# Optimization experiments

Measured on AMD Instinct MI355X. Metric: run time of the kernel, lower is better.

Reference implementation:

```python
import jax, jax.numpy as jnp
import numpy as np
import math

D_MODEL = 512
NHEAD = 8
DH = D_MODEL // NHEAD
TEMP = math.sqrt(D_MODEL / NHEAD)
EPS = 1e-5


def setup_inputs() -> dict:
    key = jax.random.key(0)
    ks = jax.random.split(key, 16)
    d, f = D_MODEL, 2 * D_MODEL
    s = 1.0 / math.sqrt(d)
    inp = {
        "x": jax.random.normal(ks[0], (1024, 16, d), dtype=jnp.float32),
        # attention projections (stored [in, out]; y = x @ W + b)
        "Wq": jax.random.normal(ks[1], (d, d), jnp.float32) * s,
        "bq": jax.random.normal(ks[2], (d,), jnp.float32) * 0.01,
        "Wk": jax.random.normal(ks[3], (d, d), jnp.float32) * s,
        "bk": jax.random.normal(ks[4], (d,), jnp.float32) * 0.01,
        "Wv": jax.random.normal(ks[5], (d, d), jnp.float32) * s,
        "bv": jax.random.normal(ks[6], (d,), jnp.float32) * 0.01,
        # layernorms
        "g1": jnp.ones((d,), jnp.float32),
        "be1": jnp.zeros((d,), jnp.float32),
        "g2": jnp.ones((d,), jnp.float32),
        "be2": jnp.zeros((d,), jnp.float32),
        # FFN
        "W1": jax.random.normal(ks[7], (d, f), jnp.float32) * s,
        "bf1": jax.random.normal(ks[8], (f,), jnp.float32) * 0.01,
        "W2": jax.random.normal(ks[9], (f, d), jnp.float32) * (1.0 / math.sqrt(f)),
        "bf2": jax.random.normal(ks[10], (d,), jnp.float32) * 0.01,
    }
    return inp


def _ln(x, g, b):
    m = jnp.mean(x, axis=-1, keepdims=True)
    v = jnp.var(x, axis=-1, keepdims=True)
    return (x - m) * jax.lax.rsqrt(v + EPS) * g + b


def reference(x, Wq, bq, Wk, bk, Wv, bv, g1, be1, g2, be2, W1, bf1, W2, bf2):
    A, B, d = x.shape
    x = _ln(x, g1, be1)                       # [A,B,d]
    # project then move batch axis first: [B,A,H,dh] -> [B,H,A,dh]
    def proj(W, b):
        y = jnp.swapaxes(x @ W + b, 0, 1)      # [B,A,d]
        return y.reshape(B, A, NHEAD, DH).transpose(0, 2, 1, 3)
    q, k, v = proj(Wq, bq), proj(Wk, bk), proj(Wv, bv)
    scores = jnp.einsum("bhqd,bhkd->bhqk", q, k)          # [B,H,A,A]
    # per-head global std over (B,A,A), unbiased (torch.std default ddof=1)
    std = jnp.std(scores, axis=(0, 2, 3), ddof=1)          # [H]
    scaling = TEMP * jnp.sqrt(1.0 + std)                   # [H]
    attn = jax.nn.softmax(scores / scaling[None, :, None, None], axis=-1)
    out = jnp.einsum("bhqk,bhkd->bhqd", attn, v)           # [B,H,A,dh]
    out = jnp.swapaxes(out.transpose(0, 2, 1, 3).reshape(B, A, d), 0, 1)  # [A,B,d]
    xt = _ln(x + out, g2, be2)
    h = jax.nn.gelu(xt @ W1 + bf1, approximate=False)      # exact GELU (torch default)
    return xt + h @ W2 + bf2
```

## Files before the change

### kernel.cpp

```cpp
#include <hip/hip_runtime.h>
#include <stdint.h>

typedef unsigned short u16;
typedef u16 u16x4 __attribute__((ext_vector_type(4)));
typedef unsigned int u32x4 __attribute__((ext_vector_type(4)));
typedef float f32x4 __attribute__((ext_vector_type(4)));
typedef float f32x16 __attribute__((ext_vector_type(16)));
typedef __bf16 bf16x8 __attribute__((ext_vector_type(8)));

#define DEVI __device__ __forceinline__

DEVI u16 f2bf(float f) {
  uint32_t u = __builtin_bit_cast(uint32_t, f);
  u = (u + 0x7FFFu + ((u >> 16) & 1u)) >> 16;
  return (u16)u;
}
DEVI float bf2f(u16 h) {
  uint32_t u = ((uint32_t)h) << 16;
  return __builtin_bit_cast(float, u);
}
DEVI f32x4 mfma16(u32x4 a, u32x4 b, f32x4 c) {
  return __builtin_amdgcn_mfma_f32_16x16x32_bf16(
      __builtin_bit_cast(bf16x8, a), __builtin_bit_cast(bf16x8, b), c, 0, 0, 0);
}
DEVI f32x16 mfma32(u32x4 a, u32x4 b, f32x16 c) {
  return __builtin_amdgcn_mfma_f32_32x32x16_bf16(
      __builtin_bit_cast(bf16x8, a), __builtin_bit_cast(bf16x8, b), c, 0, 0, 0);
}
DEVI uint32_t cvtpk(float lo, float hi) {
  uint32_t w;
  asm("v_cvt_pk_bf16_f32 %0, %1, %2" : "=v"(w) : "v"(lo), "v"(hi));
  return w;
}
DEVI void plswap(uint32_t& a, uint32_t& b) {
  asm("v_permlane32_swap_b32 %0, %1" : "+v"(a), "+v"(b));
}
DEVI float xmax2(float v) {
  uint32_t a = __builtin_bit_cast(uint32_t, v), b = a;
  plswap(a, b);
  return fmaxf(__builtin_bit_cast(float, a), __builtin_bit_cast(float, b));
}

#define AS1 __attribute__((address_space(1)))
#define AS3 __attribute__((address_space(3)))
DEVI void gload16(const void* g, void* l) {
  __builtin_amdgcn_global_load_lds((AS1 void*)(uintptr_t)g,
                                   (AS3 void*)(uint32_t)(uintptr_t)l, 16, 0, 0);
}

DEVI float wred(float v) {
#pragma unroll
  for (int m = 1; m < 64; m <<= 1) v += __shfl_xor(v, m);
  return v;
}

__global__ __launch_bounds__(256) void k_prep_ln1(
    const float* __restrict__ Wq, const float* __restrict__ Wk,
    const float* __restrict__ Wv, const float* __restrict__ W1,
    const float* __restrict__ W2, const float* __restrict__ x,
    const float* __restrict__ gam, const float* __restrict__ bet,
    u16* __restrict__ wqkv_t, u16* __restrict__ w1t, u16* __restrict__ w2t,
    u16* __restrict__ xn_res) {
  __shared__ float tile[64][65];
  int bid = blockIdx.x, tid = threadIdx.x;
  if (bid < 448) {
    const float* W;
    u16* Wt;
    int Kr, Nc, n0, k0;
    if (bid < 192) {
      int w = bid / 64, t = bid & 63;
      W = (w == 0) ? Wq : (w == 1) ? Wk : Wv;
      Wt = wqkv_t + (size_t)w * 512 * 512;
      Kr = 512; Nc = 512; n0 = (t & 7) * 64; k0 = (t >> 3) * 64;
    } else if (bid < 320) {
      int t = bid - 192;
      W = W1; Wt = w1t;
      Kr = 512; Nc = 1024; n0 = (t & 15) * 64; k0 = (t >> 4) * 64;
    } else {
      int t = bid - 320;
      W = W2; Wt = w2t;
      Kr = 1024; Nc = 512; n0 = (t & 7) * 64; k0 = (t >> 3) * 64;
    }
#pragma unroll
    for (int i = 0; i < 16; i++) {
      int idx = i * 256 + tid;
      int r = idx >> 6, cc = idx & 63;
      tile[r][cc] = W[(size_t)(k0 + r) * Nc + n0 + cc];
    }
    __syncthreads();
#pragma unroll
    for (int i = 0; i < 16; i++) {
      int idx = i * 256 + tid;
      int r = idx >> 6, cc = idx & 63;
      Wt[(size_t)(n0 + r) * Kr + k0 + cc] = f2bf(tile[cc][r]);
    }
  } else {
    int wid = tid >> 6, lane = tid & 63;
    int row = (bid - 448) * 4 + wid;
    const float* xr = x + (size_t)row * 512 + lane * 8;
    f32x4 v0 = *(const f32x4*)xr;
    f32x4 v1 = *(const f32x4*)(xr + 4);
    float s = 0.f, ss = 0.f;
#pragma unroll
    for (int j = 0; j < 4; j++) {
      s += v0[j] + v1[j];
      ss += v0[j] * v0[j] + v1[j] * v1[j];
    }
    s = wred(s);
    ss = wred(ss);
    float mean = s * (1.0f / 512.0f);
    float var = ss * (1.0f / 512.0f) - mean * mean;
    float rstd = rsqrtf(var + 1e-5f);
    const float* gp = gam + lane * 8;
    const float* bp = bet + lane * 8;
    f32x4 ga = *(const f32x4*)gp, gb = *(const f32x4*)(gp + 4);
    f32x4 ba = *(const f32x4*)bp, bb = *(const f32x4*)(bp + 4);
    u16x4 o0, o1;
#pragma unroll
    for (int j = 0; j < 4; j++) {
      o0[j] = f2bf((v0[j] - mean) * rstd * ga[j] + ba[j]);
      o1[j] = f2bf((v1[j] - mean) * rstd * gb[j] + bb[j]);
    }
    u16* pr = xn_res + (size_t)row * 512 + lane * 8;
    *(u16x4*)pr = o0;
    *(u16x4*)(pr + 4) = o1;
  }
}

__global__ __launch_bounds__(256) void k_ln2(const u16* __restrict__ xn,
                                             const u16* __restrict__ ao,
                                             const float* __restrict__ gam,
                                             const float* __restrict__ bet,
                                             u16* __restrict__ xt) {
  int tid = threadIdx.x, wid = tid >> 6, lane = tid & 63;
  int row = blockIdx.x * 4 + wid;
  size_t base = (size_t)row * 512 + lane * 8;
  u16x4 a0 = *(const u16x4*)&xn[base], a1 = *(const u16x4*)&xn[base + 4];
  u16x4 c0 = *(const u16x4*)&ao[base], c1 = *(const u16x4*)&ao[base + 4];
  float v[8];
#pragma unroll
  for (int j = 0; j < 4; j++) {
    v[j] = bf2f(a0[j]) + bf2f(c0[j]);
    v[4 + j] = bf2f(a1[j]) + bf2f(c1[j]);
  }
  float s = 0.f, ss = 0.f;
#pragma unroll
  for (int j = 0; j < 8; j++) {
    s += v[j];
    ss += v[j] * v[j];
  }
  s = wred(s);
  ss = wred(ss);
  float mean = s * (1.0f / 512.0f);
  float var = ss * (1.0f / 512.0f) - mean * mean;
  float rstd = rsqrtf(var + 1e-5f);
  const float* gp = gam + lane * 8;
  const float* bp = bet + lane * 8;
  u16x4 o0, o1;
#pragma unroll
  for (int j = 0; j < 4; j++) {
    o0[j] = f2bf((v[j] - mean) * rstd * gp[j] + bp[j]);
    o1[j] = f2bf((v[4 + j] - mean) * rstd * gp[4 + j] + bp[4 + j]);
  }
  u16* pr = xt + base;
  *(u16x4*)pr = o0;
  *(u16x4*)(pr + 4) = o1;
}

template <int EPI, int BM>
__global__ __launch_bounds__(256, BM == 64 ? 4 : 3) void k_gemm(
    const u16* __restrict__ A, const u16* __restrict__ B, int K,
    const float* __restrict__ b0, const float* __restrict__ b1,
    const float* __restrict__ b2, u16* __restrict__ o0, u16* __restrict__ o1,
    u16* __restrict__ o2, u16* __restrict__ qt, u16* __restrict__ kt,
    const u16* __restrict__ resid, float* __restrict__ outf) {
  constexpr int MI = BM / 64;
  __shared__ __align__(16) u16 As[BM * 64];
  __shared__ __align__(16) u16 Bs[128 * 64];
  const int tid = threadIdx.x;
  const int wid = tid >> 6, lane = tid & 63;
  const int r31 = lane & 31, hi = lane >> 5;
  const int m0 = blockIdx.x * BM, n0 = blockIdx.y * 128;
  const int wr = (wid >> 1) * (BM / 2), wc = (wid & 1) * 64;
  const int srow = tid >> 3, scb = tid & 7;

  f32x16 acc[MI][2];
#pragma unroll
  for (int i = 0; i < MI; i++)
#pragma unroll
    for (int j = 0; j < 2; j++)
#pragma unroll
      for (int e = 0; e < 16; e++) acc[i][j][e] = 0.f;

  auto stage = [&](int k0) {
#pragma unroll
    for (int i = 0; i < BM / 32; i++) {
      int row = i * 32 + srow;
      int col = ((scb ^ (row & 7)) << 3);
      const u16* asrc;
      if constexpr (EPI == 0) {
        int m = m0 + row;
        asrc = A + ((size_t)(((m & 1023) << 4) | (m >> 10))) * K + k0 + col;
      } else {
        asrc = A + (size_t)(m0 + row) * K + k0 + col;
      }
      gload16(asrc, &As[(i * 256 + tid) * 8]);
    }
#pragma unroll
    for (int i = 0; i < 4; i++) {
      int row = i * 32 + srow;
      int col = ((scb ^ (row & 7)) << 3);
      gload16(B + (size_t)(n0 + row) * K + k0 + col, &Bs[(i * 256 + tid) * 8]);
    }
  };

  for (int k0 = 0; k0 < K; k0 += 64) {
    __syncthreads();
    stage(k0);
    __syncthreads();
#pragma unroll
    for (int kk = 0; kk < 4; kk++) {
      u32x4 af[MI], bfr[2];
#pragma unroll
      for (int mi = 0; mi < MI; mi++) {
        int row = wr + mi * 32 + r31;
        int cb = (kk * 2 + hi) ^ (row & 7);
        af[mi] = *(const u32x4*)&As[row * 64 + cb * 8];
      }
#pragma unroll
      for (int ni = 0; ni < 2; ni++) {
        int row = wc + ni * 32 + r31;
        int cb = (kk * 2 + hi) ^ (row & 7);
        bfr[ni] = *(const u32x4*)&Bs[row * 64 + cb * 8];
      }
#pragma unroll
      for (int mi = 0; mi < MI; mi++)
#pragma unroll
        for (int ni = 0; ni < 2; ni++)
          acc[mi][ni] = mfma32(af[mi], bfr[ni], acc[mi][ni]);
    }
  }

  if constexpr (EPI == 0) {
#pragma unroll
    for (int mi = 0; mi < MI; mi++) {
#pragma unroll
      for (int ni = 0; ni < 2; ni++) {
        int n = n0 + wc + ni * 32 + r31;
        int which = n >> 9, h = (n >> 6) & 7, dh = n & 63;
        const float* bp = (which == 0) ? b0 : (which == 1) ? b1 : b2;
        float bias = bp[n & 511];
#pragma unroll
        for (int grp = 0; grp < 4; grp++) {
          int mbase = m0 + wr + mi * 32 + grp * 8 + hi * 4;
          int bb = mbase >> 10, aa = mbase & 1023;
          int bh = bb * 8 + h;
          u16x4 pk;
#pragma unroll
          for (int j = 0; j < 4; j++) pk[j] = f2bf(acc[mi][ni][grp * 4 + j] + bias);
          if (which < 2) {
            u16* dstr = ((which == 0) ? o0 : o1) + ((size_t)bh * 1024 + aa) * 64 + dh;
#pragma unroll
            for (int j = 0; j < 4; j++) dstr[(size_t)j * 64] = pk[j];
            u16* dstt = ((which == 0) ? qt : kt) + ((size_t)bh * 64 + dh) * 1024 + aa;
            *(u16x4*)dstt = pk;
          } else {
            *(u16x4*)(o2 + ((size_t)bh * 64 + dh) * 1024 + aa) = pk;
          }
        }
      }
    }
  } else if constexpr (EPI == 1) {
#pragma unroll
    for (int mi = 0; mi < MI; mi++) {
#pragma unroll
      for (int ni = 0; ni < 2; ni++) {
        int n = n0 + wc + ni * 32 + r31;
        float bias = b0[n];
#pragma unroll
        for (int i = 0; i < 16; i++) {
          int m = m0 + wr + mi * 32 + (i & 3) + 8 * (i >> 2) + 4 * hi;
          float v = acc[mi][ni][i] + bias;
          v = 0.5f * v * (1.0f + erff(v * 0.70710678118654752f));
          o0[(size_t)m * 1024 + n] = f2bf(v);
        }
      }
    }
  } else {
#pragma unroll
    for (int mi = 0; mi < MI; mi++) {
#pragma unroll
      for (int ni = 0; ni < 2; ni++) {
        int n = n0 + wc + ni * 32 + r31;
        float bias = b0[n];
#pragma unroll
        for (int i = 0; i < 16; i++) {
          int m = m0 + wr + mi * 32 + (i & 3) + 8 * (i >> 2) + 4 * hi;
          float v = acc[mi][ni][i] + bias + bf2f(resid[(size_t)m * 512 + n]);
          outf[(size_t)m * 512 + n] = v;
        }
      }
    }
  }
}

__global__ __launch_bounds__(256) void k_gram2(const u16* __restrict__ qt,
                                               const u16* __restrict__ kt,
                                               float* __restrict__ stats) {
  __shared__ __align__(16) u16 Xq[2][64 * 64];
  __shared__ __align__(16) u16 Xk[2][64 * 64];
  __shared__ float red[8];
  int tid = threadIdx.x, wid = tid >> 6, lane = tid & 63;
  int g = lane >> 4, c = lane & 15;
  int bh = blockIdx.x;
  const int srow = tid >> 3, scb = tid & 7;
  const u32x4 ones = {0x3F803F80u, 0x3F803F80u, 0x3F803F80u, 0x3F803F80u};
  const f32x4 zero = {0.f, 0.f, 0.f, 0.f};
  const u16* qsrc = qt + ((size_t)bh << 16);
  const u16* ksrc = kt + ((size_t)bh << 16);

  f32x4 gq[4], gk[4], csq = zero, csk = zero;
#pragma unroll
  for (int j = 0; j < 4; j++) {
    gq[j] = zero;
    gk[j] = zero;
  }

  auto stage = [&](int buf, int k0) {
#pragma unroll
    for (int i = 0; i < 2; i++) {
      int row = i * 32 + srow;
      int col = ((scb ^ (row & 7)) << 3);
      gload16(qsrc + (size_t)row * 1024 + k0 + col, &Xq[buf][(i * 256 + tid) * 8]);
      gload16(ksrc + (size_t)row * 1024 + k0 + col, &Xk[buf][(i * 256 + tid) * 8]);
    }
  };

  stage(0, 0);
  int cur = 0;
  for (int k0 = 0; k0 < 1024; k0 += 64) {
    __syncthreads();
    if (k0 + 64 < 1024) stage(cur ^ 1, k0 + 64);
#pragma unroll
    for (int kk = 0; kk < 2; kk++) {
      int arow = wid * 16 + c;
      int cba = (kk * 4 + g) ^ (arow & 7);
      u32x4 aq = *(const u32x4*)&Xq[cur][arow * 64 + cba * 8];
      u32x4 ak = *(const u32x4*)&Xk[cur][arow * 64 + cba * 8];
      csq = mfma16(aq, ones, csq);
      csk = mfma16(ak, ones, csk);
#pragma unroll
      for (int ni = 0; ni < 4; ni++) {
        int brow = ni * 16 + c;
        int cbb = (kk * 4 + g) ^ (brow & 7);
        u32x4 bq = *(const u32x4*)&Xq[cur][brow * 64 + cbb * 8];
        u32x4 bk = *(const u32x4*)&Xk[cur][brow * 64 + cbb * 8];
        gq[ni] = mfma16(aq, bq, gq[ni]);
        gk[ni] = mfma16(ak, bk, gk[ni]);
      }
    }
    cur ^= 1;
  }
  float part = 0.f;
#pragma unroll
  for (int ni = 0; ni < 4; ni++)
#pragma unroll
    for (int r = 0; r < 4; r++) part += gq[ni][r] * gk[ni][r];
  part = wred(part);
  float cpart = 0.f;
  if (c == 0) {
#pragma unroll
    for (int r = 0; r < 4; r++) cpart += csq[r] * csk[r];
  }
  cpart = wred(cpart);
  if (lane == 0) {
    red[wid] = part;
    red[4 + wid] = cpart;
  }
  __syncthreads();
  if (tid == 0) {
    stats[bh * 2] = red[0] + red[1] + red[2] + red[3];
    stats[bh * 2 + 1] = red[4] + red[5] + red[6] + red[7];
  }
}

__global__ __launch_bounds__(256, 3) void k_attn(const u16* __restrict__ q,
                                                 const u16* __restrict__ k,
                                                 const u16* __restrict__ vt,
                                                 const float* __restrict__ stats,
                                                 u16* __restrict__ ao) {
  __shared__ __align__(16) u16 Ks[2][64 * 64];
  __shared__ __align__(16) u16 Vs[2][64 * 64];
  int tid = threadIdx.x, wid = tid >> 6, lane = tid & 63;
  int r = lane & 31, hi = lane >> 5, h8 = hi * 8;
  int bh = blockIdx.x, qt = blockIdx.y;
  int b = bh >> 3, h = bh & 7;
  float ssq = 0.f, sm = 0.f;
#pragma unroll
  for (int bb2 = 0; bb2 < 16; bb2++) {
    ssq += stats[(bb2 * 8 + h) * 2];
    sm += stats[(bb2 * 8 + h) * 2 + 1];
  }
  const float NN = 16777216.0f;
  float var = (ssq - sm * sm / NN) / (NN - 1.0f);
  float sd = sqrtf(fmaxf(var, 0.0f));
  float sc = 1.4426950408889634f / (8.0f * sqrtf(1.0f + sd));
  int q0 = qt * 128 + wid * 32;
  const u16* qb = q + ((size_t)bh << 16);
  const u16* kb = k + ((size_t)bh << 16);
  const u16* vb = vt + ((size_t)bh << 16);
  const int srow = tid >> 3, scb = tid & 7;
  const u32x4 ones = {0x3F803F80u, 0x3F803F80u, 0x3F803F80u, 0x3F803F80u};

  u32x4 qf[4];
  const u16* qrow = qb + (size_t)(q0 + r) * 64 + h8;
#pragma unroll
  for (int ks = 0; ks < 4; ks++) {
    u32x4 raw = *(const u32x4*)(qrow + ks * 16);
    u32x4 w;
#pragma unroll
    for (int t = 0; t < 4; t++) {
      float lo = bf2f((u16)(raw[t] & 0xffffu)) * sc;
      float hi_ = bf2f((u16)(raw[t] >> 16)) * sc;
      w[t] = cvtpk(lo, hi_);
    }
    qf[ks] = w;
  }

  const f32x16 zero16 = {0.f, 0.f, 0.f, 0.f, 0.f, 0.f, 0.f, 0.f,
                         0.f, 0.f, 0.f, 0.f, 0.f, 0.f, 0.f, 0.f};
  f32x16 o0 = zero16, o1 = zero16, lacc = zero16;
  float m_run = -1e30f;

  auto stage = [&](int buf, int t0) {
#pragma unroll
    for (int i = 0; i < 2; i++) {
      int row = i * 32 + srow;
      int col = ((scb ^ (row & 7)) << 3);
      gload16(kb + (size_t)(t0 + row) * 64 + col, &Ks[buf][(i * 256 + tid) * 8]);
      gload16(vb + (size_t)row * 1024 + t0 + col, &Vs[buf][(i * 256 + tid) * 8]);
    }
  };

  stage(0, 0);
  int cur = 0;
  for (int t0 = 0; t0 < 1024; t0 += 64) {
    __syncthreads();
    if (t0 + 64 < 1024) stage(cur ^ 1, t0 + 64);
    const u16* Kc = Ks[cur];
    const u16* Vc = Vs[cur];
#pragma unroll
    for (int ss = 0; ss < 2; ss++) {
      f32x16 st = zero16;
      int rk = ss * 32 + r;
      __builtin_amdgcn_s_setprio(1);
#pragma unroll
      for (int ks = 0; ks < 4; ks++) {
        int cb = (ks * 2 + hi) ^ (rk & 7);
        u32x4 kf = *(const u32x4*)&Kc[rk * 64 + cb * 8];
        st = mfma32(kf, qf[ks], st);
      }
      __builtin_amdgcn_s_setprio(0);
      float mx[8];
#pragma unroll
      for (int i = 0; i < 8; i++) mx[i] = fmaxf(st[i], st[i + 8]);
#pragma unroll
      for (int i = 0; i < 4; i++) mx[i] = fmaxf(mx[i], mx[i + 4]);
      float pm = fmaxf(fmaxf(mx[0], mx[2]), fmaxf(mx[1], mx[3]));
      pm = xmax2(pm);
      if (__any(pm > m_run + 8.0f)) {
        float mnew = fmaxf(m_run, pm);
        float al = exp2f(m_run - mnew);
        lacc[0] *= al;
#pragma unroll
        for (int i = 0; i < 16; i++) {
          o0[i] *= al;
          o1[i] *= al;
        }
        m_run = mnew;
      }
      float p[16];
#pragma unroll
      for (int i = 0; i < 16; i++) p[i] = exp2f(st[i] - m_run);
      __builtin_amdgcn_s_setprio(1);
#pragma unroll
      for (int ks = 0; ks < 2; ks++) {
        uint32_t A0 = cvtpk(p[ks * 8 + 0], p[ks * 8 + 1]);
        uint32_t A1 = cvtpk(p[ks * 8 + 4], p[ks * 8 + 5]);
        plswap(A0, A1);
        uint32_t B0 = cvtpk(p[ks * 8 + 2], p[ks * 8 + 3]);
        uint32_t B1 = cvtpk(p[ks * 8 + 6], p[ks * 8 + 7]);
        plswap(B0, B1);
        u32x4 pa = {A0, B0, A1, B1};
        lacc = mfma32(ones, pa, lacc);
#pragma unroll
        for (int mt = 0; mt < 2; mt++) {
          int rv = mt * 32 + r;
          int cb = (ss * 4 + ks * 2 + hi) ^ (rv & 7);
          u32x4 vf = *(const u32x4*)&Vc[rv * 64 + cb * 8];
          if (mt == 0)
            o0 = mfma32(vf, pa, o0);
          else
            o1 = mfma32(vf, pa, o1);
        }
      }
      __builtin_amdgcn_s_setprio(0);
    }
    cur ^= 1;
  }

  float inv = 1.0f / lacc[0];
  int a_idx = q0 + r;
  u16* aop = ao + ((size_t)(a_idx * 16 + b)) * 512 + h * 64;
#pragma unroll
  for (int i = 0; i < 16; i++) {
    int dh0 = (i & 3) + 8 * (i >> 2) + 4 * hi;
    aop[dh0] = f2bf(o0[i] * inv);
    aop[32 + dh0] = f2bf(o1[i] * inv);
  }
}

extern "C" void kernel_launch(void* const* d_in, const int* in_sizes, int n_in,
                              void* d_out, int out_size, void* d_ws, size_t ws_size,
                              hipStream_t stream) {
  const float* x = (const float*)d_in[0];
  const float* Wq = (const float*)d_in[1];
  const float* bq = (const float*)d_in[2];
  const float* Wk = (const float*)d_in[3];
  const float* bk = (const float*)d_in[4];
  const float* Wv = (const float*)d_in[5];
  const float* bv = (const float*)d_in[6];
  const float* g1 = (const float*)d_in[7];
  const float* be1 = (const float*)d_in[8];
  const float* g2 = (const float*)d_in[9];
  const float* be2 = (const float*)d_in[10];
  const float* W1 = (const float*)d_in[11];
  const float* bf1 = (const float*)d_in[12];
  const float* W2 = (const float*)d_in[13];
  const float* bf2v = (const float*)d_in[14];
  float* out = (float*)d_out;

  char* w = (char*)d_ws;
  size_t off = 0;
  auto alloc = [&](size_t bytes) -> void* {
    void* p = w + off;
    off += (bytes + 255) & ~(size_t)255;
    return p;
  };
  u16* xn_res = (u16*)alloc(16384ull * 512 * 2);
  u16* qbuf = (u16*)alloc(128ull * 1024 * 64 * 2);
  u16* kbuf = (u16*)alloc(128ull * 1024 * 64 * 2);
  u16* vtb = (u16*)alloc(128ull * 64 * 1024 * 2);
  u16* qtb = (u16*)alloc(128ull * 64 * 1024 * 2);
  u16* ktb = (u16*)alloc(128ull * 64 * 1024 * 2);
  u16* wqkv_t = (u16*)alloc(1536ull * 512 * 2);
  u16* w1t = (u16*)alloc(1024ull * 512 * 2);
  u16* w2t = (u16*)alloc(512ull * 1024 * 2);
  u16* h_bf = (u16*)alloc(16384ull * 1024 * 2);
  float* stats = (float*)alloc(128ull * 2 * 4);
  u16* ao_bf = (u16*)alloc(16384ull * 512 * 2);
  u16* xt_bf = (u16*)alloc(16384ull * 512 * 2);

  k_prep_ln1<<<448 + 4096, 256, 0, stream>>>(Wq, Wk, Wv, W1, W2, x, g1, be1,
                                             wqkv_t, w1t, w2t, xn_res);

  k_gemm<0, 128><<<dim3(128, 12), 256, 0, stream>>>(
      xn_res, wqkv_t, 512, bq, bk, bv, qbuf, kbuf, vtb, qtb, ktb, nullptr,
      nullptr);

  k_gram2<<<128, 256, 0, stream>>>(qtb, ktb, stats);

  k_attn<<<dim3(128, 8), 256, 0, stream>>>(qbuf, kbuf, vtb, stats, ao_bf);

  k_ln2<<<4096, 256, 0, stream>>>(xn_res, ao_bf, g2, be2, xt_bf);

  k_gemm<1, 128><<<dim3(128, 8), 256, 0, stream>>>(
      xt_bf, w1t, 512, bf1, nullptr, nullptr, h_bf, nullptr, nullptr, nullptr,
      nullptr, nullptr, nullptr);
  k_gemm<2, 64><<<dim3(256, 4), 256, 0, stream>>>(
      h_bf, w2t, 1024, bf2v, nullptr, nullptr, nullptr, nullptr, nullptr,
      nullptr, nullptr, xt_bf, out);
  (void)in_sizes; (void)n_in; (void)out_size; (void)ws_size;
}
```

Measured before the change: 214.1 us.

## Process two query tiles per attention wave and remap GEMM blocks across XCDs

The attention kernel now has each wave handle two 32-row query tiles. Each K fragment loaded from LDS is reused for two QK^T MFMAs, and each V fragment for two PV MFMAs. The grid is halved and occupancy lowered to 2 blocks per CU to make room for the extra accumulators. The GEMMs switch to a 1D grid with an XCD-aware block remap, so consecutive tiles share the L2 on one XCD. exp2f is also replaced by the hardware exp2 builtin. The attention change trades more registers and fewer resident waves for less LDS traffic per MFMA.

```diff
diff --git a/kernel.cpp b/kernel.cpp
--- a/kernel.cpp
+++ b/kernel.cpp
@@ -40,6 +40,7 @@
   plswap(a, b);
   return fmaxf(__builtin_bit_cast(float, a), __builtin_bit_cast(float, b));
 }
+DEVI float ex2(float x) { return __builtin_amdgcn_exp2f(x); }
 
 #define AS1 __attribute__((address_space(1)))
 #define AS3 __attribute__((address_space(3)))
@@ -167,9 +168,9 @@
   *(u16x4*)(pr + 4) = o1;
 }
 
-template <int EPI, int BM>
+template <int EPI, int BM, int NB>
 __global__ __launch_bounds__(256, BM == 64 ? 4 : 3) void k_gemm(
-    const u16* __restrict__ A, const u16* __restrict__ B, int K,
+    const u16* __restrict__ A, const u16* __restrict__ B, int K, int nwg8,
     const float* __restrict__ b0, const float* __restrict__ b1,
     const float* __restrict__ b2, u16* __restrict__ o0, u16* __restrict__ o1,
     u16* __restrict__ o2, u16* __restrict__ qt, u16* __restrict__ kt,
@@ -180,7 +181,9 @@
   const int tid = threadIdx.x;
   const int wid = tid >> 6, lane = tid & 63;
   const int r31 = lane & 31, hi = lane >> 5;
-  const int m0 = blockIdx.x * BM, n0 = blockIdx.y * 128;
+  const int bid = blockIdx.x;
+  const int oid = (bid & 7) * nwg8 + (bid >> 3);
+  const int m0 = (oid / NB) * BM, n0 = (oid % NB) * 128;
   const int wr = (wid >> 1) * (BM / 2), wc = (wid & 1) * 64;
   const int srow = tid >> 3, scb = tid & 7;
 
@@ -384,7 +387,42 @@
   }
 }
 
-__global__ __launch_bounds__(256, 3) void k_attn(const u16* __restrict__ q,
+DEVI void softmax_tile(const f32x16& st, float& m_run, f32x16& oa, f32x16& ob,
+                       f32x16& lacc, float* p) {
+  float mx[8];
+#pragma unroll
+  for (int i = 0; i < 8; i++) mx[i] = fmaxf(st[i], st[i + 8]);
+#pragma unroll
+  for (int i = 0; i < 4; i++) mx[i] = fmaxf(mx[i], mx[i + 4]);
+  float pm = fmaxf(fmaxf(mx[0], mx[2]), fmaxf(mx[1], mx[3]));
+  pm = xmax2(pm);
+  if (__any(pm > m_run + 8.0f)) {
+    float mnew = fmaxf(m_run, pm);
+    float al = ex2(m_run - mnew);
+    lacc[0] *= al;
+#pragma unroll
+    for (int i = 0; i < 16; i++) {
+      oa[i] *= al;
+      ob[i] *= al;
+    }
+    m_run = mnew;
+  }
+#pragma unroll
+  for (int i = 0; i < 16; i++) p[i] = ex2(st[i] - m_run);
+}
+
+DEVI u32x4 packp(const float* p, int ks) {
+  uint32_t A0 = cvtpk(p[ks * 8 + 0], p[ks * 8 + 1]);
+  uint32_t A1 = cvtpk(p[ks * 8 + 4], p[ks * 8 + 5]);
+  plswap(A0, A1);
+  uint32_t B0 = cvtpk(p[ks * 8 + 2], p[ks * 8 + 3]);
+  uint32_t B1 = cvtpk(p[ks * 8 + 6], p[ks * 8 + 7]);
+  plswap(B0, B1);
+  u32x4 pa = {A0, B0, A1, B1};
+  return pa;
+}
+
+__global__ __launch_bounds__(256, 2) void k_attn(const u16* __restrict__ q,
                                                  const u16* __restrict__ k,
                                                  const u16* __restrict__ vt,
                                                  const float* __restrict__ stats,
@@ -405,32 +443,39 @@
   float var = (ssq - sm * sm / NN) / (NN - 1.0f);
   float sd = sqrtf(fmaxf(var, 0.0f));
   float sc = 1.4426950408889634f / (8.0f * sqrtf(1.0f + sd));
-  int q0 = qt * 128 + wid * 32;
+  int q0 = qt * 256 + wid * 32;
   const u16* qb = q + ((size_t)bh << 16);
   const u16* kb = k + ((size_t)bh << 16);
   const u16* vb = vt + ((size_t)bh << 16);
   const int srow = tid >> 3, scb = tid & 7;
   const u32x4 ones = {0x3F803F80u, 0x3F803F80u, 0x3F803F80u, 0x3F803F80u};
 
-  u32x4 qf[4];
-  const u16* qrow = qb + (size_t)(q0 + r) * 64 + h8;
-#pragma unroll
-  for (int ks = 0; ks < 4; ks++) {
-    u32x4 raw = *(const u32x4*)(qrow + ks * 16);
-    u32x4 w;
-#pragma unroll
-    for (int t = 0; t < 4; t++) {
-      float lo = bf2f((u16)(raw[t] & 0xffffu)) * sc;
-      float hi_ = bf2f((u16)(raw[t] >> 16)) * sc;
-      w[t] = cvtpk(lo, hi_);
-    }
-    qf[ks] = w;
+  u32x4 qf1[4], qf2[4];
+#pragma unroll
+  for (int tt = 0; tt < 2; tt++) {
+    const u16* qrow = qb + (size_t)(q0 + tt * 128 + r) * 64 + h8;
+#pragma unroll
+    for (int ks = 0; ks < 4; ks++) {
+      u32x4 raw = *(const u32x4*)(qrow + ks * 16);
+      u32x4 w;
+#pragma unroll
+      for (int t = 0; t < 4; t++) {
+        float lo = bf2f((u16)(raw[t] & 0xffffu)) * sc;
+        float hi_ = bf2f((u16)(raw[t] >> 16)) * sc;
+        w[t] = cvtpk(lo, hi_);
+      }
+      if (tt == 0)
+        qf1[ks] = w;
+      else
+        qf2[ks] = w;
+    }
   }
 
   const f32x16 zero16 = {0.f, 0.f, 0.f, 0.f, 0.f, 0.f, 0.f, 0.f,
                          0.f, 0.f, 0.f, 0.f, 0.f, 0.f, 0.f, 0.f};
-  f32x16 o0 = zero16, o1 = zero16, lacc = zero16;
-  float m_run = -1e30f;
+  f32x16 o0 = zero16, o1 = zero16, o2 = zero16, o3 = zero16;
+  f32x16 lacc1 = zero16, lacc2 = zero16;
+  float m1 = -1e30f, m2 = -1e30f;
 
   auto stage = [&](int buf, int t0) {
 #pragma unroll
@@ -451,57 +496,42 @@
     const u16* Vc = Vs[cur];
 #pragma unroll
     for (int ss = 0; ss < 2; ss++) {
-      f32x16 st = zero16;
       int rk = ss * 32 + r;
-      __builtin_amdgcn_s_setprio(1);
+      u32x4 kf[4];
 #pragma unroll
       for (int ks = 0; ks < 4; ks++) {
         int cb = (ks * 2 + hi) ^ (rk & 7);
-        u32x4 kf = *(const u32x4*)&Kc[rk * 64 + cb * 8];
-        st = mfma32(kf, qf[ks], st);
-      }
+        kf[ks] = *(const u32x4*)&Kc[rk * 64 + cb * 8];
+      }
+      f32x16 st1 = zero16, st2 = zero16;
+      __builtin_amdgcn_s_setprio(1);
+#pragma unroll
+      for (int ks = 0; ks < 4; ks++) st1 = mfma32(kf[ks], qf1[ks], st1);
+#pragma unroll
+      for (int ks = 0; ks < 4; ks++) st2 = mfma32(kf[ks], qf2[ks], st2);
       __builtin_amdgcn_s_setprio(0);
-      float mx[8];
-#pragma unroll
-      for (int i = 0; i < 8; i++) mx[i] = fmaxf(st[i], st[i + 8]);
-#pragma unroll
-      for (int i = 0; i < 4; i++) mx[i] = fmaxf(mx[i], mx[i + 4]);
-      float pm = fmaxf(fmaxf(mx[0], mx[2]), fmaxf(mx[1], mx[3]));
-      pm = xmax2(pm);
-      if (__any(pm > m_run + 8.0f)) {
-        float mnew = fmaxf(m_run, pm);
-        float al = exp2f(m_run - mnew);
-        lacc[0] *= al;
-#pragma unroll
-        for (int i = 0; i < 16; i++) {
-          o0[i] *= al;
-          o1[i] *= al;
-        }
-        m_run = mnew;
-      }
-      float p[16];
-#pragma unroll
-      for (int i = 0; i < 16; i++) p[i] = exp2f(st[i] - m_run);
+      float p1[16], p2[16];
+      softmax_tile(st1, m1, o0, o1, lacc1, p1);
+      softmax_tile(st2, m2, o2, o3, lacc2, p2);
       __builtin_amdgcn_s_setprio(1);
 #pragma unroll
       for (int ks = 0; ks < 2; ks++) {
-        uint32_t A0 = cvtpk(p[ks * 8 + 0], p[ks * 8 + 1]);
-        uint32_t A1 = cvtpk(p[ks * 8 + 4], p[ks * 8 + 5]);
-        plswap(A0, A1);
-        uint32_t B0 = cvtpk(p[ks * 8 + 2], p[ks * 8 + 3]);
-        uint32_t B1 = cvtpk(p[ks * 8 + 6], p[ks * 8 + 7]);
-        plswap(B0, B1);
-        u32x4 pa = {A0, B0, A1, B1};
-        lacc = mfma32(ones, pa, lacc);
+        u32x4 pa1 = packp(p1, ks);
+        u32x4 pa2 = packp(p2, ks);
+        lacc1 = mfma32(ones, pa1, lacc1);
+        lacc2 = mfma32(ones, pa2, lacc2);
 #pragma unroll
         for (int mt = 0; mt < 2; mt++) {
           int rv = mt * 32 + r;
           int cb = (ss * 4 + ks * 2 + hi) ^ (rv & 7);
           u32x4 vf = *(const u32x4*)&Vc[rv * 64 + cb * 8];
-          if (mt == 0)
-            o0 = mfma32(vf, pa, o0);
-          else
-            o1 = mfma32(vf, pa, o1);
+          if (mt == 0) {
+            o0 = mfma32(vf, pa1, o0);
+            o2 = mfma32(vf, pa2, o2);
+          } else {
+            o1 = mfma32(vf, pa1, o1);
+            o3 = mfma32(vf, pa2, o3);
+          }
         }
       }
       __builtin_amdgcn_s_setprio(0);
@@ -509,14 +539,24 @@
     cur ^= 1;
   }
 
-  float inv = 1.0f / lacc[0];
-  int a_idx = q0 + r;
-  u16* aop = ao + ((size_t)(a_idx * 16 + b)) * 512 + h * 64;
-#pragma unroll
-  for (int i = 0; i < 16; i++) {
-    int dh0 = (i & 3) + 8 * (i >> 2) + 4 * hi;
-    aop[dh0] = f2bf(o0[i] * inv);
-    aop[32 + dh0] = f2bf(o1[i] * inv);
+  float inv1 = 1.0f / lacc1[0];
+  float inv2 = 1.0f / lacc2[0];
+#pragma unroll
+  for (int tt = 0; tt < 2; tt++) {
+    int a_idx = q0 + tt * 128 + r;
+    u16* aop = ao + ((size_t)(a_idx * 16 + b)) * 512 + h * 64;
+    float inv = tt == 0 ? inv1 : inv2;
+#pragma unroll
+    for (int i = 0; i < 16; i++) {
+      int dh0 = (i & 3) + 8 * (i >> 2) + 4 * hi;
+      if (tt == 0) {
+        aop[dh0] = f2bf(o0[i] * inv);
+        aop[32 + dh0] = f2bf(o1[i] * inv);
+      } else {
+        aop[dh0] = f2bf(o2[i] * inv);
+        aop[32 + dh0] = f2bf(o3[i] * inv);
+      }
+    }
   }
 }
 
@@ -564,21 +604,21 @@
   k_prep_ln1<<<448 + 4096, 256, 0, stream>>>(Wq, Wk, Wv, W1, W2, x, g1, be1,
                                              wqkv_t, w1t, w2t, xn_res);
 
-  k_gemm<0, 128><<<dim3(128, 12), 256, 0, stream>>>(
-      xn_res, wqkv_t, 512, bq, bk, bv, qbuf, kbuf, vtb, qtb, ktb, nullptr,
+  k_gemm<0, 128, 12><<<1536, 256, 0, stream>>>(
+      xn_res, wqkv_t, 512, 192, bq, bk, bv, qbuf, kbuf, vtb, qtb, ktb, nullptr,
       nullptr);
 
   k_gram2<<<128, 256, 0, stream>>>(qtb, ktb, stats);
 
-  k_attn<<<dim3(128, 8), 256, 0, stream>>>(qbuf, kbuf, vtb, stats, ao_bf);
+  k_attn<<<dim3(128, 4), 256, 0, stream>>>(qbuf, kbuf, vtb, stats, ao_bf);
 
   k_ln2<<<4096, 256, 0, stream>>>(xn_res, ao_bf, g2, be2, xt_bf);
 
-  k_gemm<1, 128><<<dim3(128, 8), 256, 0, stream>>>(
-      xt_bf, w1t, 512, bf1, nullptr, nullptr, h_bf, nullptr, nullptr, nullptr,
-      nullptr, nullptr, nullptr);
-  k_gemm<2, 64><<<dim3(256, 4), 256, 0, stream>>>(
-      h_bf, w2t, 1024, bf2v, nullptr, nullptr, nullptr, nullptr, nullptr,
+  k_gemm<1, 128, 8><<<1024, 256, 0, stream>>>(
+      xt_bf, w1t, 512, 128, bf1, nullptr, nullptr, h_bf, nullptr, nullptr,
+      nullptr, nullptr, nullptr, nullptr);
+  k_gemm<2, 64, 4><<<1024, 256, 0, stream>>>(
+      h_bf, w2t, 1024, 128, bf2v, nullptr, nullptr, nullptr, nullptr, nullptr,
       nullptr, nullptr, xt_bf, out);
   (void)in_sizes; (void)n_in; (void)out_size; (void)ws_size;
 }
```

Result: faster. 201.4 us (-5.9%).
